# Performance work log

Hardware: AMD Instinct MI355X
Metric: run time of the kernel (lower is better)

Reference implementation:

```python
import jax, jax.numpy as jnp
import numpy as np

B, H, W, DIM, WS, NH, HID = 16, 64, 64, 256, 8, 8, 1024
SHIFT = WS // 2
N = WS * WS  # tokens per window


def _rel_pos_index(ws):
    coords = np.stack(np.meshgrid(np.arange(ws), np.arange(ws), indexing='ij')).reshape(2, -1)
    rel = (coords[:, :, None] - coords[:, None, :]).transpose(1, 2, 0)  # [n,n,2]
    rel[..., 0] += ws - 1
    rel[..., 1] += ws - 1
    rel[..., 0] *= 2 * ws - 1
    return rel.sum(-1)  # [n,n] ints in [0, (2ws-1)^2)


def _attn_mask(h, w, ws, ss):
    img = np.zeros((h, w), np.float32)
    cnt = 0
    sl = (slice(0, -ws), slice(-ws, -ss), slice(-ss, None))
    for hs in sl:
        for wsl in sl:
            img[hs, wsl] = cnt
            cnt += 1
    mw = img.reshape(h // ws, ws, w // ws, ws).transpose(0, 2, 1, 3).reshape(-1, ws * ws)
    d = mw[:, None, :] - mw[:, :, None]  # unsqueeze(1) - unsqueeze(2)
    return np.where(d != 0, np.float32(-100.0), np.float32(0.0))  # [nW,n,n]


RPI = jnp.asarray(_rel_pos_index(WS).reshape(-1))          # [n*n] int
MASK = jnp.asarray(_attn_mask(H, W, WS, SHIFT))            # [nW,n,n]


def ln(x, g, b, eps):
    m = x.mean(-1, keepdims=True)
    v = x.var(-1, keepdims=True)
    return (x - m) / jnp.sqrt(v + eps) * g + b


def win_part(x, ws):
    b, h, w, c = x.shape
    x = x.reshape(b, h // ws, ws, w // ws, ws, c).transpose(0, 1, 3, 2, 4, 5)
    return x.reshape(-1, ws * ws, c)  # [b*nW, n, c]


def win_rev(win, ws, h, w):
    c = win.shape[-1]
    b = win.shape[0] // ((h // ws) * (w // ws))
    x = win.reshape(b, h // ws, w // ws, ws, ws, c).transpose(0, 1, 3, 2, 4, 5)
    return x.reshape(b, h, w, c)


def attention(xw, qkv_w, qkv_b, rpb, out_w, out_b, mask):
    Bw, n, c = xw.shape
    dh = c // NH
    scale = dh ** -0.5
    qkv = (xw @ qkv_w + qkv_b).reshape(Bw, n, 3, NH, dh).transpose(2, 0, 3, 1, 4)
    q, k, v = qkv[0], qkv[1], qkv[2]                       # [Bw,NH,n,dh]
    dots = jnp.einsum('bhid,bhjd->bhij', q, k) * scale
    bias = rpb[RPI].reshape(n, n, NH).transpose(2, 0, 1)   # [NH,n,n]
    attn = dots + bias[None]
    if mask is not None:
        nW = mask.shape[0]
        attn = attn.reshape(Bw // nW, nW, NH, n, n) + mask[None, :, None]
        attn = attn.reshape(Bw, NH, n, n)
    attn = jax.nn.softmax(attn, axis=-1)
    out = jnp.einsum('bhij,bhjd->bhid', attn, v)
    out = out.transpose(0, 2, 1, 3).reshape(Bw, n, c)
    return out @ out_w + out_b


def block(x, shifted, mask, n1g, n1b, qkv_w, qkv_b, rpb, out_w, out_b,
          n2g, n2b, lng, lnb, w1, b1, w2, b2):
    b, l, c = x.shape
    shortcut = x
    x = ln(x, n1g, n1b, 1e-5).reshape(b, H, W, c)
    if shifted:
        x = jnp.roll(x, (-SHIFT, -SHIFT), (1, 2))
    xw = win_part(x, WS)
    xw = attention(xw, qkv_w, qkv_b, rpb, out_w, out_b, mask)
    x = win_rev(xw, WS, H, W)
    if shifted:
        x = jnp.roll(x, (SHIFT, SHIFT), (1, 2))
    x = shortcut + x.reshape(b, l, c)
    # FeedForward contains its own LayerNorm(eps=1e-6) after norm2 (faithful to source)
    h = ln(x, n2g, n2b, 1e-5)
    h = ln(h, lng, lnb, 1e-6)
    h = jax.nn.gelu(h @ w1 + b1, approximate=False) @ w2 + b2
    return x + h


def forward(x, *p):
    x = block(x, False, None, *p[0:15])
    x = block(x, True, MASK, *p[15:30])
    return x


def setup_inputs() -> dict:
    key = jax.random.key(0)
    ks = iter(jax.random.split(key, 16))
    s = 0.02
    d = {'x': jax.random.normal(next(ks), (B, H * W, DIM), jnp.float32)}
    for i in (0, 1):
        p = f'b{i}_'
        d[p + 'n1g'] = jnp.ones((DIM,), jnp.float32)
        d[p + 'n1b'] = jnp.zeros((DIM,), jnp.float32)
        d[p + 'qkv_w'] = jax.random.normal(next(ks), (DIM, 3 * DIM), jnp.float32) * s
        d[p + 'qkv_b'] = jnp.zeros((3 * DIM,), jnp.float32)
        d[p + 'rpb'] = jax.random.normal(next(ks), ((2 * WS - 1) ** 2, NH), jnp.float32) * s
        d[p + 'out_w'] = jax.random.normal(next(ks), (DIM, DIM), jnp.float32) * s
        d[p + 'out_b'] = jnp.zeros((DIM,), jnp.float32)
        d[p + 'n2g'] = jnp.ones((DIM,), jnp.float32)
        d[p + 'n2b'] = jnp.zeros((DIM,), jnp.float32)
        d[p + 'lng'] = jnp.ones((DIM,), jnp.float32)
        d[p + 'lnb'] = jnp.zeros((DIM,), jnp.float32)
        d[p + 'w1'] = jax.random.normal(next(ks), (DIM, HID), jnp.float32) * s
        d[p + 'b1'] = jnp.zeros((HID,), jnp.float32)
        d[p + 'w2'] = jax.random.normal(next(ks), (HID, DIM), jnp.float32) * s
        d[p + 'b2'] = jnp.zeros((DIM,), jnp.float32)
    return d


def reference(x,
              b0_n1g, b0_n1b, b0_qkv_w, b0_qkv_b, b0_rpb, b0_out_w, b0_out_b,
              b0_n2g, b0_n2b, b0_lng, b0_lnb, b0_w1, b0_b1, b0_w2, b0_b2,
              b1_n1g, b1_n1b, b1_qkv_w, b1_qkv_b, b1_rpb, b1_out_w, b1_out_b,
              b1_n2g, b1_n2b, b1_lng, b1_lnb, b1_w1, b1_b1, b1_w2, b1_b2):
    return forward(x,
                   b0_n1g, b0_n1b, b0_qkv_w, b0_qkv_b, b0_rpb, b0_out_w, b0_out_b,
                   b0_n2g, b0_n2b, b0_lng, b0_lnb, b0_w1, b0_b1, b0_w2, b0_b2,
                   b1_n1g, b1_n1b, b1_qkv_w, b1_qkv_b, b1_rpb, b1_out_w, b1_out_b,
                   b1_n2g, b1_n2b, b1_lng, b1_lnb, b1_w1, b1_b1, b1_w2, b1_b2)
```

## Files before the change

### kernel.cpp

```cpp
#include <hip/hip_runtime.h>

typedef unsigned short u16;
typedef __attribute__((ext_vector_type(8))) short bf16x8;
typedef __attribute__((ext_vector_type(8))) unsigned short u16x8;
typedef __attribute__((ext_vector_type(4))) unsigned short u16x4;
typedef __attribute__((ext_vector_type(4))) float f32x4;

__device__ inline float b2f(u16 u) {
    union { unsigned u32; float f; } x; x.u32 = ((unsigned)u) << 16; return x.f;
}
__device__ inline u16 f2b(float f) {
    union { float f; unsigned u; } x; x.f = f;
    unsigned r = x.u + 0x7fffu + ((x.u >> 16) & 1u);
    return (u16)(r >> 16);
}

__device__ inline float fast_gelu(float v) {
    float x = fabsf(v) * 0.70710678118654752f;
    float t = __builtin_amdgcn_rcpf(1.0f + 0.3275911f * x);
    float e = __expf(-x * x);
    float poly = ((((1.061405429f * t - 1.453152027f) * t + 1.421413741f) * t
                   - 0.284496736f) * t + 0.254829592f) * t;
    float erfv = 1.0f - poly * e;
    float w = copysignf(erfv, v);
    return 0.5f * v * (1.0f + w);
}

#define GLOAD_LDS16(g, l) \
    __builtin_amdgcn_global_load_lds((const __attribute__((address_space(1))) void*)(const void*)(g), \
                                     (__attribute__((address_space(3))) void*)(void*)(l), 16, 0, 0)
#define FENCE() asm volatile("" ::: "memory")

__global__ __launch_bounds__(256)
void ln_win_kernel(const float* __restrict__ x, const float* __restrict__ g,
                   const float* __restrict__ b, u16* __restrict__ xw, int shift)
{
    int wid = blockIdx.x * 4 + (threadIdx.x >> 6);
    int lane = threadIdx.x & 63;
    int win = wid >> 6, tok = wid & 63;
    int bb = win >> 6, wib = win & 63;
    int h = (((wib >> 3) << 3) + (tok >> 3) + shift) & 63;
    int w = (((wib & 7) << 3) + (tok & 7) + shift) & 63;
    size_t src = ((size_t)bb * 4096 + h * 64 + w) * 256;
    float4 v = ((const float4*)(x + src))[lane];
    float s = v.x + v.y + v.z + v.w;
    float s2 = v.x*v.x + v.y*v.y + v.z*v.z + v.w*v.w;
    for (int k = 32; k > 0; k >>= 1) { s += __shfl_xor(s, k); s2 += __shfl_xor(s2, k); }
    float mean = s * (1.f/256.f);
    float var  = s2 * (1.f/256.f) - mean*mean;
    float rs = rsqrtf(var + 1e-5f);
    int c = lane * 4;
    u16x4 o;
    o[0] = f2b((v.x - mean) * rs * g[c+0] + b[c+0]);
    o[1] = f2b((v.y - mean) * rs * g[c+1] + b[c+1]);
    o[2] = f2b((v.z - mean) * rs * g[c+2] + b[c+2]);
    o[3] = f2b((v.w - mean) * rs * g[c+3] + b[c+3]);
    *(u16x4*)(xw + (size_t)wid * 256 + c) = o;
}

__global__ __launch_bounds__(256)
void ln2_kernel(const float* __restrict__ xin,
                const float* __restrict__ g1, const float* __restrict__ b1,
                const float* __restrict__ g2, const float* __restrict__ b2,
                u16* __restrict__ out)
{
    int wid = blockIdx.x * 4 + (threadIdx.x >> 6);
    int lane = threadIdx.x & 63;
    float4 v = ((const float4*)(xin + (size_t)wid * 256))[lane];
    float s = v.x + v.y + v.z + v.w;
    float s2 = v.x*v.x + v.y*v.y + v.z*v.z + v.w*v.w;
    for (int k = 32; k > 0; k >>= 1) { s += __shfl_xor(s, k); s2 += __shfl_xor(s2, k); }
    float mean = s * (1.f/256.f);
    float var  = s2 * (1.f/256.f) - mean*mean;
    float rs = rsqrtf(var + 1e-5f);
    int c = lane * 4;
    float y0 = (v.x - mean) * rs * g1[c+0] + b1[c+0];
    float y1 = (v.y - mean) * rs * g1[c+1] + b1[c+1];
    float y2 = (v.z - mean) * rs * g1[c+2] + b1[c+2];
    float y3 = (v.w - mean) * rs * g1[c+3] + b1[c+3];
    float t = y0 + y1 + y2 + y3;
    float t2 = y0*y0 + y1*y1 + y2*y2 + y3*y3;
    for (int k = 32; k > 0; k >>= 1) { t += __shfl_xor(t, k); t2 += __shfl_xor(t2, k); }
    float m2 = t * (1.f/256.f);
    float v2 = t2 * (1.f/256.f) - m2*m2;
    float rs2 = rsqrtf(v2 + 1e-6f);
    u16x4 o;
    o[0] = f2b((y0 - m2) * rs2 * g2[c+0] + b2[c+0]);
    o[1] = f2b((y1 - m2) * rs2 * g2[c+1] + b2[c+1]);
    o[2] = f2b((y2 - m2) * rs2 * g2[c+2] + b2[c+2]);
    o[3] = f2b((y3 - m2) * rs2 * g2[c+3] + b2[c+3]);
    *(u16x4*)(out + (size_t)wid * 256 + c) = o;
}

__global__ __launch_bounds__(256)
void transpose_w(const float* __restrict__ W, u16* __restrict__ Wt, int K, int N)
{
    __shared__ float t[32][33];
    int nb = blockIdx.x * 32, kb = blockIdx.y * 32;
    int tx = threadIdx.x & 31, ty = threadIdx.x >> 5;
    #pragma unroll
    for (int r = 0; r < 32; r += 8)
        t[ty + r][tx] = W[(size_t)(kb + ty + r) * N + nb + tx];
    __syncthreads();
    #pragma unroll
    for (int r = 0; r < 32; r += 8)
        Wt[(size_t)(nb + ty + r) * K + kb + tx] = f2b(t[tx][ty + r]);
}

__global__ __launch_bounds__(256)
void build_bias(const float* __restrict__ rpb, float* __restrict__ bmT)
{
    int idx = blockIdx.x * 256 + threadIdx.x;
    int q = idx & 63, k = (idx >> 6) & 63, h = (idx >> 12) & 7, cls = idx >> 15;
    int qh = q >> 3, qw = q & 7, kh = k >> 3, kw = k & 7;
    float v = rpb[((qh - kh + 7) * 15 + (qw - kw + 7)) * 8 + h];
    int ch = cls >> 1, cw = cls & 1;
    int rq = (ch ? (qh < 4 ? 1 : 2) : 0) * 3 + (cw ? (qw < 4 ? 1 : 2) : 0);
    int rk = (ch ? (kh < 4 ? 1 : 2) : 0) * 3 + (cw ? (kw < 4 ? 1 : 2) : 0);
    if (rq != rk) v -= 100.f;
    bmT[idx] = v * 1.4426950408889634f;
}

template<int EPI>
__global__ __launch_bounds__(256, 2)
void gemm_areg(const u16* __restrict__ A, const u16* __restrict__ Bt,
               const float* __restrict__ bias, void* __restrict__ out,
               const float* __restrict__ resid, int N, int shift)
{
    constexpr int K = 256;
    __shared__ u16 Bs[2][8][64][32];
    const int tid = threadIdx.x, lane = tid & 63, wv = tid >> 6;
    const int g = lane >> 4, r = lane & 15;
    const int bid = blockIdx.x;
    const int bm = (bid & 7) * 64 + (bid >> 3);
    const int row0 = bm * 128 + wv * 32;

    bf16x8 af[2][8];
    #pragma unroll
    for (int rf = 0; rf < 2; ++rf)
        #pragma unroll
        for (int ks = 0; ks < 8; ++ks)
            af[rf][ks] = *(const bf16x8*)(A + (size_t)(row0 + rf * 16 + r) * K + ks * 32 + g * 8);

    const int NB = N >> 6;
#define STAGE(bn_, buf_) do { \
        _Pragma("unroll") \
        for (int it = 0; it < 8; ++it) { \
            const int S = it * 256 + wv * 64 + lane; \
            const int ks_ = S >> 8, col_ = (S >> 2) & 63, k8_ = S & 3; \
            GLOAD_LDS16(Bt + (size_t)((bn_) * 64 + col_) * K + ks_ * 32 + k8_ * 8, \
                        &Bs[buf_][0][0][0] + (size_t)(it * 256 + wv * 64) * 8); \
        } \
    } while (0)

    FENCE();
    STAGE(0, 0);
    for (int bn = 0; bn < NB; ++bn) {
        const int cur = bn & 1;
        if (bn + 1 < NB) { STAGE(bn + 1, cur ^ 1); }
        if (bn == 0) {
            asm volatile("s_waitcnt vmcnt(8)" ::: "memory");
        } else if (bn + 1 < NB) {
            if (EPI == 2) asm volatile("s_waitcnt vmcnt(24)" ::: "memory");
            else          asm volatile("s_waitcnt vmcnt(16)" ::: "memory");
        } else {
            if (EPI == 2) asm volatile("s_waitcnt vmcnt(16)" ::: "memory");
            else          asm volatile("s_waitcnt vmcnt(8)" ::: "memory");
        }
        __builtin_amdgcn_s_barrier();
        FENCE();
        f32x4 acc[4][2] = {};
        #pragma unroll
        for (int ks = 0; ks < 8; ++ks) {
            bf16x8 bf[4];
            #pragma unroll
            for (int cf = 0; cf < 4; ++cf)
                bf[cf] = *(const bf16x8*)(&Bs[cur][ks][cf * 16 + r][g * 8]);
            __builtin_amdgcn_s_setprio(1);
            #pragma unroll
            for (int cf = 0; cf < 4; ++cf)
                #pragma unroll
                for (int rf = 0; rf < 2; ++rf)
                    acc[cf][rf] = __builtin_amdgcn_mfma_f32_16x16x32_bf16(bf[cf], af[rf][ks], acc[cf][rf], 0, 0, 0);
            __builtin_amdgcn_s_setprio(0);
        }
        asm volatile("s_waitcnt lgkmcnt(0)" ::: "memory");
        __builtin_amdgcn_sched_barrier(0);
        __builtin_amdgcn_s_barrier();
        FENCE();
        #pragma unroll
        for (int rf = 0; rf < 2; ++rf) {
            const int row = row0 + rf * 16 + r;
            size_t orow;
            if (EPI == 2) {
                int win = row >> 6, tok = row & 63;
                int bb = win >> 6, wib = win & 63;
                int h = (((wib >> 3) << 3) + (tok >> 3) + shift) & 63;
                int w = (((wib & 7) << 3) + (tok & 7) + shift) & 63;
                orow = (size_t)bb * 4096 + h * 64 + w;
            } else {
                orow = (size_t)row;
            }
            #pragma unroll
            for (int cf = 0; cf < 4; ++cf) {
                const int colb = bn * 64 + cf * 16 + g * 4;
                const float4 bv = *(const float4*)(bias + colb);
                if (EPI == 0) {
                    u16x4 o;
                    o[0] = f2b(acc[cf][rf][0] + bv.x);
                    o[1] = f2b(acc[cf][rf][1] + bv.y);
                    o[2] = f2b(acc[cf][rf][2] + bv.z);
                    o[3] = f2b(acc[cf][rf][3] + bv.w);
                    *(u16x4*)((u16*)out + (size_t)row * N + colb) = o;
                } else if (EPI == 1) {
                    u16x4 o;
                    o[0] = f2b(fast_gelu(acc[cf][rf][0] + bv.x));
                    o[1] = f2b(fast_gelu(acc[cf][rf][1] + bv.y));
                    o[2] = f2b(fast_gelu(acc[cf][rf][2] + bv.z));
                    o[3] = f2b(fast_gelu(acc[cf][rf][3] + bv.w));
                    *(u16x4*)((u16*)out + (size_t)row * N + colb) = o;
                } else {
                    const float4 rv = *(const float4*)(resid + orow * N + colb);
                    float4 o;
                    o.x = rv.x + acc[cf][rf][0] + bv.x;
                    o.y = rv.y + acc[cf][rf][1] + bv.y;
                    o.z = rv.z + acc[cf][rf][2] + bv.z;
                    o.w = rv.w + acc[cf][rf][3] + bv.w;
                    *(float4*)((float*)out + orow * N + colb) = o;
                }
            }
        }
        FENCE();
    }
#undef STAGE
}

template<int EPI>
__global__ __launch_bounds__(256)
void gemm_k4(const u16* __restrict__ A, const u16* __restrict__ Bt,
             const float* __restrict__ bias, void* __restrict__ out,
             const float* __restrict__ resid, int M, int N, int K, int shift)
{
    __shared__ u16 As[4][128][32];
    __shared__ u16 Bs[4][128][32];
    const int tid = threadIdx.x, lane = tid & 63, wv = tid >> 6;
    const int g = lane >> 4, r = lane & 15;
    const int wr = wv >> 1, wc = wv & 1;
    const int nwg = gridDim.x * gridDim.y;
    const int lid = blockIdx.y * gridDim.x + blockIdx.x;
    const int qq = nwg >> 3, r8 = nwg & 7;
    const int xcd = lid & 7, pos = lid >> 3;
    const int nid = (xcd < r8 ? xcd * (qq + 1) : r8 * (qq + 1) + (xcd - r8) * qq) + pos;
    const int bm = nid / gridDim.x, bn = nid % gridDim.x;
    f32x4 acc[4][4] = {};
    const int arow = wv * 16 + (lane >> 2);
    const int scol = (((lane & 3) ^ ((lane >> 2) & 3) ^ ((lane >> 4) & 1)) * 8);
    const u16* gA = A + (size_t)(bm * 128 + arow) * K + scol;
    const u16* gB = Bt + (size_t)(bn * 128 + arow) * K + scol;
    const int nk = K >> 5;
    const int rc = (g ^ (r & 3) ^ ((r >> 2) & 1)) * 8;

#define STAGE(t) do { \
        u16* a_ = &As[(t) & 3][0][0]; u16* b_ = &Bs[(t) & 3][0][0]; \
        GLOAD_LDS16(gA + (size_t)(t) * 32,                    a_ + wv * 512); \
        GLOAD_LDS16(gA + (size_t)(t) * 32 + (size_t)64 * K,   a_ + 2048 + wv * 512); \
        GLOAD_LDS16(gB + (size_t)(t) * 32,                    b_ + wv * 512); \
        GLOAD_LDS16(gB + (size_t)(t) * 32 + (size_t)64 * K,   b_ + 2048 + wv * 512); \
    } while (0)

    STAGE(0);
    STAGE(1);
    for (int kt = 0; kt < nk; ++kt) {
        const int cur = kt & 3;
        if (kt + 2 < nk) {
            STAGE(kt + 2);
            asm volatile("s_waitcnt vmcnt(8)" ::: "memory");
        } else if (kt + 1 < nk) {
            asm volatile("s_waitcnt vmcnt(4)" ::: "memory");
        } else {
            asm volatile("s_waitcnt vmcnt(0)" ::: "memory");
        }
        __builtin_amdgcn_s_barrier();
        FENCE();
        bf16x8 af[4], bf[4];
        #pragma unroll
        for (int i = 0; i < 4; ++i)
            af[i] = *(const bf16x8*)(&As[cur][wr * 64 + i * 16 + r][rc]);
        #pragma unroll
        for (int j = 0; j < 4; ++j)
            bf[j] = *(const bf16x8*)(&Bs[cur][wc * 64 + j * 16 + r][rc]);
        __builtin_amdgcn_s_setprio(1);
        #pragma unroll
        for (int j = 0; j < 4; ++j)
            #pragma unroll
            for (int i = 0; i < 4; ++i)
                acc[j][i] = __builtin_amdgcn_mfma_f32_16x16x32_bf16(bf[j], af[i], acc[j][i], 0, 0, 0);
        __builtin_amdgcn_s_setprio(0);
        asm volatile("s_waitcnt lgkmcnt(0)" ::: "memory");
        __builtin_amdgcn_sched_barrier(0);
    }
#undef STAGE

    #pragma unroll
    for (int i = 0; i < 4; ++i) {
        const int row = bm * 128 + wr * 64 + i * 16 + r;
        #pragma unroll
        for (int j = 0; j < 4; ++j) {
            const int colb = bn * 128 + wc * 64 + j * 16 + g * 4;
            const float4 bv = *(const float4*)(bias + colb);
            const float4 rv = *(const float4*)(resid + (size_t)row * N + colb);
            float4 o;
            o.x = rv.x + acc[j][i][0] + bv.x;
            o.y = rv.y + acc[j][i][1] + bv.y;
            o.z = rv.z + acc[j][i][2] + bv.z;
            o.w = rv.w + acc[j][i][3] + bv.w;
            *(float4*)((float*)out + (size_t)row * N + colb) = o;
        }
    }
}

template<int SHIFTED>
__global__ __launch_bounds__(256)
void attn_mfma(const u16* __restrict__ qkv, const float* __restrict__ bmT,
               u16* __restrict__ out)
{
    __shared__ u16 pbuf[4][64 * 72];
    __shared__ u16 vbuf[4][32 * 72];
    const int tid = threadIdx.x, lane = tid & 63, wv = tid >> 6;
    const int g = lane >> 4, r = lane & 15;
    const int win = blockIdx.x;
    u16* P  = pbuf[wv];
    u16* Vt = vbuf[wv];
    const u16* base = qkv + (size_t)win * 64 * 768;
    int cls = 0;
    if (SHIFTED) {
        int wib = win & 63;
        cls = (((wib >> 3) == 7) ? 2 : 0) + (((wib & 7) == 7) ? 1 : 0);
    }
    const float sc = 0.17677669529663687f * 1.4426950408889634f;

    for (int hh = 0; hh < 2; ++hh) {
        const int h = wv * 2 + hh;
        const float* bmh = bmT + ((size_t)cls * 8 + h) * 4096;
        bf16x8 kf[4], qf[4];
        #pragma unroll
        for (int i = 0; i < 4; ++i) {
            kf[i] = *(const bf16x8*)(base + (size_t)(i * 16 + r) * 768 + 256 + h * 32 + g * 8);
            qf[i] = *(const bf16x8*)(base + (size_t)(i * 16 + r) * 768 +       h * 32 + g * 8);
        }
        #pragma unroll
        for (int d0 = 0; d0 < 32; d0 += 8) {
            u16x8 vv = *(const u16x8*)(base + (size_t)lane * 768 + 512 + h * 32 + d0);
            #pragma unroll
            for (int e = 0; e < 8; ++e) Vt[(d0 + e) * 72 + lane] = vv[e];
        }
        f32x4 acc[4][4] = {};
        #pragma unroll
        for (int i = 0; i < 4; ++i)
            #pragma unroll
            for (int j = 0; j < 4; ++j)
                acc[i][j] = __builtin_amdgcn_mfma_f32_16x16x32_bf16(kf[i], qf[j], acc[i][j], 0, 0, 0);
        #pragma unroll
        for (int i = 0; i < 4; ++i) {
            const int kb = (i * 16 + g * 4) * 64;
            #pragma unroll
            for (int j = 0; j < 4; ++j) {
                const int qq = j * 16 + r;
                #pragma unroll
                for (int rr = 0; rr < 4; ++rr)
                    acc[i][j][rr] = acc[i][j][rr] * sc + bmh[kb + rr * 64 + qq];
            }
        }
        float inv_[4];
        #pragma unroll
        for (int j = 0; j < 4; ++j) {
            float m = acc[0][j][0];
            #pragma unroll
            for (int i = 0; i < 4; ++i)
                #pragma unroll
                for (int rr = 0; rr < 4; ++rr) m = fmaxf(m, acc[i][j][rr]);
            m = fmaxf(m, __shfl_xor(m, 16));
            m = fmaxf(m, __shfl_xor(m, 32));
            float s = 0.f;
            #pragma unroll
            for (int i = 0; i < 4; ++i)
                #pragma unroll
                for (int rr = 0; rr < 4; ++rr) {
                    float p = exp2f(acc[i][j][rr] - m);
                    acc[i][j][rr] = p; s += p;
                }
            s += __shfl_xor(s, 16);
            s += __shfl_xor(s, 32);
            inv_[j] = 1.f / s;
        }
        #pragma unroll
        for (int j = 0; j < 4; ++j) {
            const float iv = inv_[j];
            #pragma unroll
            for (int i = 0; i < 4; ++i) {
                u16x4 w;
                #pragma unroll
                for (int rr = 0; rr < 4; ++rr) w[rr] = f2b(acc[i][j][rr] * iv);
                *(u16x4*)(P + (j * 16 + r) * 72 + i * 16 + g * 4) = w;
            }
        }
        f32x4 o[2][4] = {};
        #pragma unroll
        for (int ks = 0; ks < 2; ++ks) {
            bf16x8 pa[4], vb[2];
            #pragma unroll
            for (int i = 0; i < 4; ++i)
                pa[i] = *(const bf16x8*)(P + (i * 16 + r) * 72 + ks * 32 + g * 8);
            #pragma unroll
            for (int j = 0; j < 2; ++j)
                vb[j] = *(const bf16x8*)(Vt + (j * 16 + r) * 72 + ks * 32 + g * 8);
            #pragma unroll
            for (int j = 0; j < 2; ++j)
                #pragma unroll
                for (int i = 0; i < 4; ++i)
                    o[j][i] = __builtin_amdgcn_mfma_f32_16x16x32_bf16(vb[j], pa[i], o[j][i], 0, 0, 0);
        }
        u16* op = out + (size_t)win * 64 * 256 + h * 32;
        #pragma unroll
        for (int i = 0; i < 4; ++i) {
            const int qrow = i * 16 + r;
            #pragma unroll
            for (int j = 0; j < 2; ++j) {
                u16x4 w;
                #pragma unroll
                for (int rr = 0; rr < 4; ++rr) w[rr] = f2b(o[j][i][rr]);
                *(u16x4*)(op + (size_t)qrow * 256 + j * 16 + g * 4) = w;
            }
        }
    }
}

extern "C" void kernel_launch(void* const* d_in, const int* in_sizes, int n_in,
                              void* d_out, int out_size, void* d_ws, size_t ws_size,
                              hipStream_t stream)
{
    (void)in_sizes; (void)n_in; (void)out_size; (void)ws_size;
    const float* x = (const float*)d_in[0];
    char* ws = (char*)d_ws;
    size_t off = 0;
    auto alloc = [&](size_t bytes) { void* p = ws + off; off += (bytes + 255) & ~(size_t)255; return p; };

    u16 *wtq[2], *wto[2], *wt1[2], *wt2[2];
    float* bmT[2];
    for (int i = 0; i < 2; ++i) {
        wtq[i] = (u16*)alloc((size_t)768 * 256 * 2);
        wto[i] = (u16*)alloc((size_t)256 * 256 * 2);
        wt1[i] = (u16*)alloc((size_t)1024 * 256 * 2);
        wt2[i] = (u16*)alloc((size_t)256 * 1024 * 2);
        bmT[i] = (float*)alloc((size_t)4 * 8 * 64 * 64 * 4);
    }
    u16*  xw  = (u16*)alloc((size_t)65536 * 256 * 2);
    u16*  big = (u16*)alloc((size_t)65536 * 1024 * 2);
    float* x1 = (float*)alloc((size_t)65536 * 256 * 4);
    float* outp = (float*)d_out;

    for (int blk = 0; blk < 2; ++blk) {
        const float* const* P = (const float* const*)(d_in + 1 + blk * 15);
        transpose_w<<<dim3(768 / 32, 256 / 32), 256, 0, stream>>>(P[2], wtq[blk], 256, 768);
        transpose_w<<<dim3(256 / 32, 256 / 32), 256, 0, stream>>>(P[5], wto[blk], 256, 256);
        transpose_w<<<dim3(1024 / 32, 256 / 32), 256, 0, stream>>>(P[11], wt1[blk], 256, 1024);
        transpose_w<<<dim3(256 / 32, 1024 / 32), 256, 0, stream>>>(P[13], wt2[blk], 1024, 256);
        build_bias<<<512, 256, 0, stream>>>(P[4], bmT[blk]);
    }

    for (int blk = 0; blk < 2; ++blk) {
        const float* const* P = (const float* const*)(d_in + 1 + blk * 15);
        const int sh = blk ? 4 : 0;
        const float* xin = blk ? outp : x;

        ln_win_kernel<<<16384, 256, 0, stream>>>(xin, P[0], P[1], xw, sh);
        gemm_areg<0><<<512, 256, 0, stream>>>(xw, wtq[blk], P[3], big, nullptr, 768, 0);
        if (blk) attn_mfma<1><<<1024, 256, 0, stream>>>(big, bmT[blk], xw);
        else     attn_mfma<0><<<1024, 256, 0, stream>>>(big, bmT[blk], xw);
        gemm_areg<2><<<512, 256, 0, stream>>>(xw, wto[blk], P[6], x1, xin, 256, sh);
        ln2_kernel<<<16384, 256, 0, stream>>>(x1, P[7], P[8], P[9], P[10], xw);
        gemm_areg<1><<<512, 256, 0, stream>>>(xw, wt1[blk], P[12], big, nullptr, 1024, 0);
        gemm_k4<3><<<dim3(2, 512), 256, 0, stream>>>(big, wt2[blk], P[14], outp, x1, 65536, 256, 1024, 0);
    }
}
```

Measured before the change: 701.1 us.

## Swizzle B tile in LDS, use tanh-sigmoid GELU and library bf16 rounding

Applies an XOR swizzle to the 16-byte chunks of the B tile staged in LDS by the A-register GEMM, and applies the same swizzle on the read side, to cut LDS bank conflicts on the bf16x8 fragment loads. Replaces the erf-polynomial GELU with a tanh-style approximation written as v*sigmoid(u), which needs fewer instructions but differs slightly from exact erf GELU. Swaps the hand-written round-to-nearest-even bf16 conversion for the HIP library conversion. Also renames the kernel, removes the unused template parameter of gemm_k4 and vectorizes the epilogues.

```diff
diff --git a/kernel.cpp b/kernel.cpp
--- a/kernel.cpp
+++ b/kernel.cpp
@@ -1,4 +1,5 @@
 #include <hip/hip_runtime.h>
+#include <hip/hip_bf16.h>
 
 typedef unsigned short u16;
 typedef __attribute__((ext_vector_type(8))) short bf16x8;
@@ -10,20 +11,12 @@
     union { unsigned u32; float f; } x; x.u32 = ((unsigned)u) << 16; return x.f;
 }
 __device__ inline u16 f2b(float f) {
-    union { float f; unsigned u; } x; x.f = f;
-    unsigned r = x.u + 0x7fffu + ((x.u >> 16) & 1u);
-    return (u16)(r >> 16);
+    return __builtin_bit_cast(u16, __float2bfloat16(f));
 }
 
 __device__ inline float fast_gelu(float v) {
-    float x = fabsf(v) * 0.70710678118654752f;
-    float t = __builtin_amdgcn_rcpf(1.0f + 0.3275911f * x);
-    float e = __expf(-x * x);
-    float poly = ((((1.061405429f * t - 1.453152027f) * t + 1.421413741f) * t
-                   - 0.284496736f) * t + 0.254829592f) * t;
-    float erfv = 1.0f - poly * e;
-    float w = copysignf(erfv, v);
-    return 0.5f * v * (1.0f + w);
+    float u = v * (1.5957691216f + 0.0713548163f * v * v);
+    return v * __builtin_amdgcn_rcpf(1.0f + __expf(-u));
 }
 
 #define GLOAD_LDS16(g, l) \
@@ -123,7 +116,7 @@
 
 template<int EPI>
 __global__ __launch_bounds__(256, 2)
-void gemm_areg(const u16* __restrict__ A, const u16* __restrict__ Bt,
+void areg_gemm(const u16* __restrict__ A, const u16* __restrict__ Bt,
                const float* __restrict__ bias, void* __restrict__ out,
                const float* __restrict__ resid, int N, int shift)
 {
@@ -147,11 +140,14 @@
         _Pragma("unroll") \
         for (int it = 0; it < 8; ++it) { \
             const int S = it * 256 + wv * 64 + lane; \
-            const int ks_ = S >> 8, col_ = (S >> 2) & 63, k8_ = S & 3; \
+            const int ks_ = S >> 8, col_ = (S >> 2) & 63; \
+            const int k8_ = (S & 3) ^ (col_ & 3) ^ ((col_ >> 2) & 1); \
             GLOAD_LDS16(Bt + (size_t)((bn_) * 64 + col_) * K + ks_ * 32 + k8_ * 8, \
                         &Bs[buf_][0][0][0] + (size_t)(it * 256 + wv * 64) * 8); \
         } \
     } while (0)
+
+    const int rc = (g ^ (r & 3) ^ ((r >> 2) & 1)) * 8;
 
     FENCE();
     STAGE(0, 0);
@@ -175,7 +171,7 @@
             bf16x8 bf[4];
             #pragma unroll
             for (int cf = 0; cf < 4; ++cf)
-                bf[cf] = *(const bf16x8*)(&Bs[cur][ks][cf * 16 + r][g * 8]);
+                bf[cf] = *(const bf16x8*)(&Bs[cur][ks][cf * 16 + r][rc]);
             __builtin_amdgcn_s_setprio(1);
             #pragma unroll
             for (int cf = 0; cf < 4; ++cf)
@@ -204,29 +200,23 @@
             #pragma unroll
             for (int cf = 0; cf < 4; ++cf) {
                 const int colb = bn * 64 + cf * 16 + g * 4;
-                const float4 bv = *(const float4*)(bias + colb);
+                const f32x4 bv = *(const f32x4*)(bias + colb);
                 if (EPI == 0) {
                     u16x4 o;
-                    o[0] = f2b(acc[cf][rf][0] + bv.x);
-                    o[1] = f2b(acc[cf][rf][1] + bv.y);
-                    o[2] = f2b(acc[cf][rf][2] + bv.z);
-                    o[3] = f2b(acc[cf][rf][3] + bv.w);
+                    #pragma unroll
+                    for (int e = 0; e < 4; ++e) o[e] = f2b(acc[cf][rf][e] + bv[e]);
                     *(u16x4*)((u16*)out + (size_t)row * N + colb) = o;
                 } else if (EPI == 1) {
                     u16x4 o;
-                    o[0] = f2b(fast_gelu(acc[cf][rf][0] + bv.x));
-                    o[1] = f2b(fast_gelu(acc[cf][rf][1] + bv.y));
-                    o[2] = f2b(fast_gelu(acc[cf][rf][2] + bv.z));
-                    o[3] = f2b(fast_gelu(acc[cf][rf][3] + bv.w));
+                    #pragma unroll
+                    for (int e = 0; e < 4; ++e) o[e] = f2b(fast_gelu(acc[cf][rf][e] + bv[e]));
                     *(u16x4*)((u16*)out + (size_t)row * N + colb) = o;
                 } else {
-                    const float4 rv = *(const float4*)(resid + orow * N + colb);
-                    float4 o;
-                    o.x = rv.x + acc[cf][rf][0] + bv.x;
-                    o.y = rv.y + acc[cf][rf][1] + bv.y;
-                    o.z = rv.z + acc[cf][rf][2] + bv.z;
-                    o.w = rv.w + acc[cf][rf][3] + bv.w;
-                    *(float4*)((float*)out + orow * N + colb) = o;
+                    const f32x4 rv = *(const f32x4*)(resid + orow * N + colb);
+                    f32x4 o;
+                    #pragma unroll
+                    for (int e = 0; e < 4; ++e) o[e] = rv[e] + acc[cf][rf][e] + bv[e];
+                    *(f32x4*)((float*)out + orow * N + colb) = o;
                 }
             }
         }
@@ -235,11 +225,10 @@
 #undef STAGE
 }
 
-template<int EPI>
 __global__ __launch_bounds__(256)
 void gemm_k4(const u16* __restrict__ A, const u16* __restrict__ Bt,
-             const float* __restrict__ bias, void* __restrict__ out,
-             const float* __restrict__ resid, int M, int N, int K, int shift)
+             const float* __restrict__ bias, float* __restrict__ out,
+             const float* __restrict__ resid, int M, int N, int K)
 {
     __shared__ u16 As[4][128][32];
     __shared__ u16 Bs[4][128][32];
@@ -307,14 +296,12 @@
         #pragma unroll
         for (int j = 0; j < 4; ++j) {
             const int colb = bn * 128 + wc * 64 + j * 16 + g * 4;
-            const float4 bv = *(const float4*)(bias + colb);
-            const float4 rv = *(const float4*)(resid + (size_t)row * N + colb);
-            float4 o;
-            o.x = rv.x + acc[j][i][0] + bv.x;
-            o.y = rv.y + acc[j][i][1] + bv.y;
-            o.z = rv.z + acc[j][i][2] + bv.z;
-            o.w = rv.w + acc[j][i][3] + bv.w;
-            *(float4*)((float*)out + (size_t)row * N + colb) = o;
+            const f32x4 bv = *(const f32x4*)(bias + colb);
+            const f32x4 rv = *(const f32x4*)(resid + (size_t)row * N + colb);
+            f32x4 o;
+            #pragma unroll
+            for (int e = 0; e < 4; ++e) o[e] = rv[e] + acc[j][i][e] + bv[e];
+            *(f32x4*)(out + (size_t)row * N + colb) = o;
         }
     }
 }
@@ -474,12 +461,12 @@
         const float* xin = blk ? outp : x;
 
         ln_win_kernel<<<16384, 256, 0, stream>>>(xin, P[0], P[1], xw, sh);
-        gemm_areg<0><<<512, 256, 0, stream>>>(xw, wtq[blk], P[3], big, nullptr, 768, 0);
+        areg_gemm<0><<<512, 256, 0, stream>>>(xw, wtq[blk], P[3], big, nullptr, 768, 0);
         if (blk) attn_mfma<1><<<1024, 256, 0, stream>>>(big, bmT[blk], xw);
         else     attn_mfma<0><<<1024, 256, 0, stream>>>(big, bmT[blk], xw);
-        gemm_areg<2><<<512, 256, 0, stream>>>(xw, wto[blk], P[6], x1, xin, 256, sh);
+        areg_gemm<2><<<512, 256, 0, stream>>>(xw, wto[blk], P[6], x1, xin, 256, sh);
         ln2_kernel<<<16384, 256, 0, stream>>>(x1, P[7], P[8], P[9], P[10], xw);
-        gemm_areg<1><<<512, 256, 0, stream>>>(xw, wt1[blk], P[12], big, nullptr, 1024, 0);
-        gemm_k4<3><<<dim3(2, 512), 256, 0, stream>>>(big, wt2[blk], P[14], outp, x1, 65536, 256, 1024, 0);
-    }
-}
+        areg_gemm<1><<<512, 256, 0, stream>>>(xw, wt1[blk], P[12], big, nullptr, 1024, 0);
+        gemm_k4<<<dim3(2, 512), 256, 0, stream>>>(big, wt2[blk], P[14], outp, x1, 65536, 256, 1024);
+    }
+}
```

Result: faster. 686.3 us, median of 2 (-2.1%).
